# Kernel optimization log

Measured on AMD Instinct MI355X. Metric: run time of the kernel, lower is better.

Reference implementation:

```python
import jax, jax.numpy as jnp
import numpy as np

B, T, D, HD = 4, 4096, 1024, 64

def setup_inputs() -> dict:
    key = jax.random.key(0)
    kx, kq, kk, kv = jax.random.split(key, 4)
    s = 1.0 / np.sqrt(D)
    return {
        "x": jax.random.normal(kx, (B, T, D), dtype=jnp.float32),
        "wq": jax.random.uniform(kq, (HD, D), jnp.float32, -s, s),
        "wk": jax.random.uniform(kk, (HD, D), jnp.float32, -s, s),
        "wv": jax.random.uniform(kv, (HD, D), jnp.float32, -s, s),
    }

def reference(x, wq, wk, wv):
    # Linear(D, headDim, bias=False): y = x @ W.T with W of shape [headDim, D]
    Q = jnp.einsum('btD,dD->btd', x, wq)
    K = jnp.einsum('bsD,dD->bsd', x, wk)
    V = jnp.einsum('bsD,dD->bsd', x, wv)
    head_dim = wq.shape[0]
    logits = jnp.einsum('btd,bsd->bts', Q, K) / jnp.sqrt(jnp.float32(head_dim))
    attn = jax.nn.softmax(logits, axis=-1)
    return jnp.einsum('bts,bsd->btd', attn, V)
```

## Files before the change

### kernel.cpp

```cpp
#include <hip/hip_runtime.h>
#include <math.h>

#define TLEN 4096
#define BD   1024
#define HDIM 64
#define NB   4

typedef __attribute__((ext_vector_type(8))) short bf16x8;
typedef __attribute__((ext_vector_type(4))) float f32x4;
typedef __attribute__((ext_vector_type(16))) float f32x16;

__device__ __forceinline__ unsigned short f2bf(float f) {
    union { float f; unsigned u; } v; v.f = f;
    unsigned r = v.u + 0x7FFF + ((v.u >> 16) & 1);
    return (unsigned short)(r >> 16);
}

__device__ __forceinline__ unsigned cvt_pk_bf16(float lo, float hi) {
    unsigned r;
    asm("v_cvt_pk_bf16_f32 %0, %1, %2" : "=v"(r) : "v"(lo), "v"(hi));
    return r;
}

__device__ __forceinline__ bf16x8 cvt8pk(const float4 a, const float4 b) {
    union { unsigned u[4]; bf16x8 v; } r;
    r.u[0] = cvt_pk_bf16(a.x, a.y);
    r.u[1] = cvt_pk_bf16(a.z, a.w);
    r.u[2] = cvt_pk_bf16(b.x, b.y);
    r.u[3] = cvt_pk_bf16(b.z, b.w);
    return r.v;
}

__global__ __launch_bounds__(256) void wconv_kernel(
    const float* __restrict__ wq, const float* __restrict__ wk,
    const float* __restrict__ wv, unsigned short* __restrict__ wbf)
{
    const int r = blockIdx.x;
    const float* src = (r < 64) ? wq : (r < 128) ? wk : wv;
    const int rr = r & 63;
    const int c  = threadIdx.x * 4;
    float4 a = *(const float4*)&src[(size_t)rr * BD + c];
    uint2 o;
    o.x = cvt_pk_bf16(a.x, a.y);
    o.y = cvt_pk_bf16(a.z, a.w);
    *(uint2*)&wbf[(size_t)r * BD + c] = o;
}

__global__ __launch_bounds__(256, 2) void qkv_kernel(
    const float* __restrict__ x,
    const unsigned short* __restrict__ wbf,
    unsigned short* __restrict__ Qb,
    unsigned short* __restrict__ Kb,
    unsigned short* __restrict__ Vt)
{
    const int r0   = blockIdx.x * 32;
    const int tid  = threadIdx.x;
    const int lane = tid & 63;
    const int w    = tid >> 6;
    const int g    = lane >> 4;
    const int c    = lane & 15;

    __shared__ __align__(16) unsigned short wsh[2][192 * 64];
    __shared__ __align__(16) unsigned short xh[2][32 * 64];
    __shared__ __align__(16) unsigned short vtr[64][40];

    f32x4 acc[3][2];
    #pragma unroll
    for (int t = 0; t < 3; ++t)
        #pragma unroll
        for (int rg = 0; rg < 2; ++rg) acc[t][rg] = (f32x4){0.f, 0.f, 0.f, 0.f};

    uint4 wreg[6], xreg[2];
    const int xrow = tid >> 3;
    const int xpch = tid & 7;
    const int xgch = xpch ^ (xrow & 7);

    #define LOAD_W(k0s)                                                         \
        {                                                                       \
            _Pragma("unroll")                                                   \
            for (int ii = 0; ii < 6; ++ii) {                                    \
                const int L   = ii * 256 + tid;                                 \
                const int row = L >> 3;                                         \
                const int jl  = (L & 7) ^ (row & 7);                            \
                wreg[ii] = *(const uint4*)&wbf[(size_t)row * BD + (k0s) + jl * 8]; \
            }                                                                   \
        }
    #define WRITE_W(buf)                                                        \
        {                                                                       \
            _Pragma("unroll")                                                   \
            for (int ii = 0; ii < 6; ++ii) {                                    \
                const int L = ii * 256 + tid;                                   \
                *(uint4*)&wsh[buf][L * 8] = wreg[ii];                           \
            }                                                                   \
        }
    #define LOAD_X(k0s)                                                         \
        {                                                                       \
            const float* xs = &x[(size_t)(r0 + xrow) * BD + (k0s) + xgch * 8];  \
            xreg[0] = *(const uint4*)&xs[0];                                    \
            xreg[1] = *(const uint4*)&xs[4];                                    \
        }
    #define WRITE_X(buf)                                                        \
        {                                                                       \
            union { uint4 u; float4 f; } a0, a1;                                \
            a0.u = xreg[0]; a1.u = xreg[1];                                     \
            *(bf16x8*)&xh[buf][xrow * 64 + xpch * 8] = cvt8pk(a0.f, a1.f);      \
        }

    LOAD_W(0)
    LOAD_X(0)
    WRITE_W(0)
    WRITE_X(0)

    for (int it = 0; it < 16; ++it) {
        const int cb = it & 1;
        __syncthreads();

        if (it < 15) {
            LOAD_W((it + 1) * 64)
            LOAD_X((it + 1) * 64)
        }

        #pragma unroll
        for (int h = 0; h < 2; ++h) {
            const int oct = h * 4 + g;
            const int slot = (oct ^ (c & 7)) * 8;
            bf16x8 aX[2], bW[3];
            #pragma unroll
            for (int rg = 0; rg < 2; ++rg) {
                const int row = rg * 16 + c;
                aX[rg] = *(const bf16x8*)&xh[cb][row * 64 + slot];
            }
            #pragma unroll
            for (int t = 0; t < 3; ++t)
                bW[t] = *(const bf16x8*)&wsh[cb][((w * 3 + t) * 16 + c) * 64 + slot];
            #pragma unroll
            for (int t = 0; t < 3; ++t)
                #pragma unroll
                for (int rg = 0; rg < 2; ++rg)
                    acc[t][rg] = __builtin_amdgcn_mfma_f32_16x16x32_bf16(
                        aX[rg], bW[t], acc[t][rg], 0, 0, 0);
        }

        if (it < 15) {
            WRITE_W(cb ^ 1)
            WRITE_X(cb ^ 1)
        }
    }

    const float qscale = 0.18033688f;
    const int   bb     = r0 / TLEN;
    const int   trow   = r0 % TLEN;
    #pragma unroll
    for (int t = 0; t < 3; ++t) {
        const int m = w * 3 + t;
        #pragma unroll
        for (int rg = 0; rg < 2; ++rg)
            #pragma unroll
            for (int i = 0; i < 4; ++i) {
                const int row = rg * 16 + g * 4 + i;
                if (m < 4)
                    Qb[(size_t)(r0 + row) * HDIM + m * 16 + c]
                        = f2bf(acc[t][rg][i] * qscale);
                else if (m < 8)
                    Kb[(size_t)(r0 + row) * HDIM + (m - 4) * 16 + c]
                        = f2bf(acc[t][rg][i]);
                else
                    vtr[(m - 8) * 16 + c][row] = f2bf(acc[t][rg][i]);
            }
    }
    __syncthreads();
    {
        const int d    = tid >> 2;
        const int part = tid & 3;
        uint4 v0 = *(const uint4*)&vtr[d][part * 8];
        unsigned short* dst = Vt + (size_t)bb * HDIM * TLEN + (size_t)d * TLEN
                            + trow + part * 8;
        *(uint4*)&dst[0] = v0;
    }
    #undef LOAD_W
    #undef WRITE_W
    #undef LOAD_X
    #undef WRITE_X
}

template <int KEYS>
__global__ __launch_bounds__(256, 2) void attn_kernel(
    const unsigned short* __restrict__ Qb,
    const unsigned short* __restrict__ Kb,
    const unsigned short* __restrict__ Vt,
    float* __restrict__ O1, float* __restrict__ Ml, float* __restrict__ out)
{
    const int b     = blockIdx.y;
    const int q0    = blockIdx.x * 128;
    const int split = blockIdx.z;
    const int sbase = split * KEYS;

    const unsigned short* Qp = Qb + (size_t)b * TLEN * HDIM;
    const unsigned short* Kp = Kb + (size_t)b * TLEN * HDIM + (size_t)sbase * HDIM;
    const unsigned short* Vp = Vt + (size_t)b * HDIM * TLEN + sbase;

    const int tid  = threadIdx.x;
    const int lane = tid & 63;
    const int w    = tid >> 6;
    const int ql   = lane & 31;
    const int hi   = lane >> 5;
    const int ch   = lane & 7;

    __shared__ __align__(16) unsigned short ksh[2][4096];
    __shared__ __align__(16) unsigned short vsh[2][4096];

    bf16x8 qB[4];
    #pragma unroll
    for (int s = 0; s < 4; ++s)
        qB[s] = *(const bf16x8*)
            &Qp[(size_t)(q0 + w * 32 + ql) * HDIM + s * 16 + hi * 8];

    float  lsum = 0.f;
    f32x16 oacc[2];
    #pragma unroll
    for (int dt = 0; dt < 2; ++dt)
        #pragma unroll
        for (int i = 0; i < 16; ++i) oacc[dt][i] = 0.f;

    const int nt = KEYS / 64;

    uint4 kreg[2], vreg[2];
    #define LOAD_KV(s0)                                                         \
        {                                                                       \
            _Pragma("unroll")                                                   \
            for (int ii = 0; ii < 2; ++ii) {                                    \
                const int L   = ii * 256 + tid;                                 \
                const int row = L >> 3;                                         \
                const int jl  = (L & 7) ^ (row & 7);                            \
                kreg[ii] = *(const uint4*)&Kp[(size_t)((s0) + row) * HDIM + jl * 8]; \
                vreg[ii] = *(const uint4*)&Vp[(size_t)row * TLEN + (s0) + jl * 8];   \
            }                                                                   \
        }
    #define WRITE_KV(buf)                                                       \
        {                                                                       \
            _Pragma("unroll")                                                   \
            for (int ii = 0; ii < 2; ++ii) {                                    \
                const int L = ii * 256 + tid;                                   \
                *(uint4*)&ksh[buf][L * 8] = kreg[ii];                           \
                *(uint4*)&vsh[buf][L * 8] = vreg[ii];                           \
            }                                                                   \
        }

    LOAD_KV(0)
    WRITE_KV(0)

    for (int it = 0; it < nt; ++it) {
        const int cb = it & 1;
        __syncthreads();

        if (it + 1 < nt) LOAD_KV((it + 1) * 64)

        f32x16 sacc[2];
        #pragma unroll
        for (int kt = 0; kt < 2; ++kt)
            #pragma unroll
            for (int i = 0; i < 16; ++i) sacc[kt][i] = 0.f;
        __builtin_amdgcn_s_setprio(1);
        #pragma unroll
        for (int kt = 0; kt < 2; ++kt)
            #pragma unroll
            for (int s = 0; s < 4; ++s) {
                const bf16x8 kA = *(const bf16x8*)
                    &ksh[cb][(32 * kt + ql) * 64 + ((2 * s + hi) ^ ch) * 8];
                sacc[kt] = __builtin_amdgcn_mfma_f32_32x32x16_bf16(
                    kA, qB[s], sacc[kt], 0, 0, 0);
            }
        __builtin_amdgcn_s_setprio(0);

        if (it + 1 < nt) WRITE_KV(cb ^ 1)

        bf16x8 paf[4];
        #pragma unroll
        for (int kt = 0; kt < 2; ++kt) {
            float p[16];
            #pragma unroll
            for (int i = 0; i < 16; ++i)
                p[i] = __builtin_amdgcn_exp2f(sacc[kt][i]);
            lsum += (((p[0] + p[1]) + (p[2] + p[3]))
                   + ((p[4] + p[5]) + (p[6] + p[7])))
                  + (((p[8] + p[9]) + (p[10] + p[11]))
                   + ((p[12] + p[13]) + (p[14] + p[15])));
            #pragma unroll
            for (int bb = 0; bb < 2; ++bb) {
                const unsigned X0 = cvt_pk_bf16(p[8 * bb + 0], p[8 * bb + 1]);
                const unsigned X1 = cvt_pk_bf16(p[8 * bb + 2], p[8 * bb + 3]);
                const unsigned Z0 = cvt_pk_bf16(p[8 * bb + 4], p[8 * bb + 5]);
                const unsigned Z1 = cvt_pk_bf16(p[8 * bb + 6], p[8 * bb + 7]);
                auto s02 = __builtin_amdgcn_permlane32_swap(X0, Z0, false, false);
                auto s13 = __builtin_amdgcn_permlane32_swap(X1, Z1, false, false);
                union { unsigned u[4]; bf16x8 v; } pu;
                pu.u[0] = s02[0]; pu.u[1] = s13[0];
                pu.u[2] = s02[1]; pu.u[3] = s13[1];
                paf[kt * 2 + bb] = pu.v;
            }
        }

        __builtin_amdgcn_s_setprio(1);
        #pragma unroll
        for (int dt = 0; dt < 2; ++dt)
            #pragma unroll
            for (int s = 0; s < 4; ++s) {
                const bf16x8 vB = *(const bf16x8*)
                    &vsh[cb][(32 * dt + ql) * 64 + ((2 * s + hi) ^ ch) * 8];
                oacc[dt] = __builtin_amdgcn_mfma_f32_32x32x16_bf16(
                    paf[s], vB, oacc[dt], 0, 0, 0);
            }
        __builtin_amdgcn_s_setprio(0);
    }
    #undef LOAD_KV
    #undef WRITE_KV

    lsum += __shfl_xor(lsum, 32);

    if (KEYS == TLEN) {
        #pragma unroll
        for (int r = 0; r < 16; ++r) {
            const int   qr   = (r & 3) + 8 * (r >> 2) + 4 * hi;
            const float inv  = 1.0f / __shfl(lsum, qr);
            const size_t orow = (size_t)b * TLEN + q0 + w * 32 + qr;
            out[orow * HDIM + ql]      = oacc[0][r] * inv;
            out[orow * HDIM + 32 + ql] = oacc[1][r] * inv;
        }
    } else {
        float* Od = (split == 0)
            ? out : O1 + (size_t)(split - 1) * NB * TLEN * HDIM;
        #pragma unroll
        for (int r = 0; r < 16; ++r) {
            const int   qr   = (r & 3) + 8 * (r >> 2) + 4 * hi;
            const size_t orow = (size_t)b * TLEN + q0 + w * 32 + qr;
            Od[orow * HDIM + ql]      = oacc[0][r];
            Od[orow * HDIM + 32 + ql] = oacc[1][r];
        }
        if (lane < 32)
            Ml[(size_t)(split * NB + b) * TLEN + q0 + w * 32 + lane] = lsum;
    }
}

__global__ __launch_bounds__(256) void merge_kernel(
    float* __restrict__ out, const float* __restrict__ O1,
    const float* __restrict__ Ml)
{
    const int idx  = blockIdx.x * 256 + threadIdx.x;
    const int row  = idx >> 4;
    const int col4 = (idx & 15) * 4;
    const int b    = row >> 12;
    const int t    = row & (TLEN - 1);
    float l = 0.f;
    #pragma unroll
    for (int s = 0; s < 4; ++s) l += Ml[(size_t)(s * NB + b) * TLEN + t];
    const float inv = 1.0f / l;
    float4 a = *(const float4*)&out[(size_t)row * HDIM + col4];
    #pragma unroll
    for (int s = 1; s < 4; ++s) {
        float4 p = *(const float4*)
            &O1[(size_t)(s - 1) * NB * TLEN * HDIM + (size_t)row * HDIM + col4];
        a.x += p.x; a.y += p.y; a.z += p.z; a.w += p.w;
    }
    a.x *= inv; a.y *= inv; a.z *= inv; a.w *= inv;
    *(float4*)&out[(size_t)row * HDIM + col4] = a;
}

extern "C" void kernel_launch(void* const* d_in, const int* in_sizes, int n_in,
                              void* d_out, int out_size, void* d_ws, size_t ws_size,
                              hipStream_t stream)
{
    (void)in_sizes; (void)n_in; (void)out_size;
    const float* x  = (const float*)d_in[0];
    const float* wq = (const float*)d_in[1];
    const float* wk = (const float*)d_in[2];
    const float* wv = (const float*)d_in[3];
    float* out = (float*)d_out;

    unsigned short* wbf = (unsigned short*)d_out;
    unsigned short* Qbf = (unsigned short*)d_ws;
    unsigned short* Kbf = Qbf + (size_t)NB * TLEN * HDIM;
    unsigned short* Vtb = Kbf + (size_t)NB * TLEN * HDIM;
    float* Ml = (float*)((char*)d_ws + (size_t)3 * NB * TLEN * HDIM * 2);
    float* O1 = Ml + (size_t)4 * NB * TLEN;
    const size_t ws_need = (size_t)3 * NB * TLEN * HDIM * 2
                         + (size_t)4 * NB * TLEN * 4
                         + (size_t)3 * NB * TLEN * HDIM * 4;
    const bool use_split = ws_size >= ws_need;

    wconv_kernel<<<dim3(192), 256, 0, stream>>>(wq, wk, wv, wbf);
    qkv_kernel<<<dim3(NB * TLEN / 32), 256, 0, stream>>>(x, wbf, Qbf, Kbf, Vtb);

    if (use_split) {
        attn_kernel<TLEN / 4><<<dim3(TLEN / 128, NB, 4), 256, 0, stream>>>(
            Qbf, Kbf, Vtb, O1, Ml, out);
        merge_kernel<<<dim3(NB * TLEN * 16 / 256), 256, 0, stream>>>(out, O1, Ml);
    } else {
        attn_kernel<TLEN><<<dim3(TLEN / 128, NB, 1), 256, 0, stream>>>(
            Qbf, Kbf, Vtb, O1, Ml, out);
    }
}
```

Baseline: 138.5 us.

## Prefetch x two stages ahead and use non-draining barrier in QKV projection

The QKV projection kernel now keeps two register sets for x tiles and issues x global loads two iterations ahead, alternating between them in a fully unrolled loop. __syncthreads is replaced by a barrier that waits only on LDS counters (lgkmcnt), so outstanding global loads are not drained at each barrier. This is meant to hide the fp32 x load latency behind more compute. In exchange it uses more registers, which could pressure occupancy at launch bounds (256,2).

Result: no change. 139.7 us (+0.8%).

```diff
diff --git a/kernel.cpp b/kernel.cpp
--- a/kernel.cpp
+++ b/kernel.cpp
@@ -29,6 +29,13 @@
     r.u[2] = cvt_pk_bf16(b.x, b.y);
     r.u[3] = cvt_pk_bf16(b.z, b.w);
     return r.v;
+}
+
+__device__ __forceinline__ void sync_nodrain() {
+    asm volatile("s_waitcnt lgkmcnt(0)" ::: "memory");
+    __builtin_amdgcn_sched_barrier(0);
+    __builtin_amdgcn_s_barrier();
+    __builtin_amdgcn_sched_barrier(0);
 }
 
 __global__ __launch_bounds__(256) void wconv_kernel(
@@ -70,7 +77,8 @@
         #pragma unroll
         for (int rg = 0; rg < 2; ++rg) acc[t][rg] = (f32x4){0.f, 0.f, 0.f, 0.f};
 
-    uint4 wreg[6], xreg[2];
+    uint4 wreg[6];
+    uint4 xA0, xA1, xB0, xB1;
     const int xrow = tid >> 3;
     const int xpch = tid & 7;
     const int xgch = xpch ^ (xrow & 7);
@@ -93,58 +101,78 @@
                 *(uint4*)&wsh[buf][L * 8] = wreg[ii];                           \
             }                                                                   \
         }
-    #define LOAD_X(k0s)                                                         \
+    #define LOAD_XA(k0s)                                                        \
         {                                                                       \
             const float* xs = &x[(size_t)(r0 + xrow) * BD + (k0s) + xgch * 8];  \
-            xreg[0] = *(const uint4*)&xs[0];                                    \
-            xreg[1] = *(const uint4*)&xs[4];                                    \
-        }
-    #define WRITE_X(buf)                                                        \
+            xA0 = *(const uint4*)&xs[0];                                        \
+            xA1 = *(const uint4*)&xs[4];                                        \
+        }
+    #define LOAD_XB(k0s)                                                        \
+        {                                                                       \
+            const float* xs = &x[(size_t)(r0 + xrow) * BD + (k0s) + xgch * 8];  \
+            xB0 = *(const uint4*)&xs[0];                                        \
+            xB1 = *(const uint4*)&xs[4];                                        \
+        }
+    #define WRITE_XA(buf)                                                       \
         {                                                                       \
             union { uint4 u; float4 f; } a0, a1;                                \
-            a0.u = xreg[0]; a1.u = xreg[1];                                     \
+            a0.u = xA0; a1.u = xA1;                                             \
             *(bf16x8*)&xh[buf][xrow * 64 + xpch * 8] = cvt8pk(a0.f, a1.f);      \
         }
+    #define WRITE_XB(buf)                                                       \
+        {                                                                       \
+            union { uint4 u; float4 f; } a0, a1;                                \
+            a0.u = xB0; a1.u = xB1;                                             \
+            *(bf16x8*)&xh[buf][xrow * 64 + xpch * 8] = cvt8pk(a0.f, a1.f);      \
+        }
+
+    #define COMPUTE(cbv)                                                        \
+        {                                                                       \
+            _Pragma("unroll")                                                   \
+            for (int h = 0; h < 2; ++h) {                                       \
+                const int oct = h * 4 + g;                                      \
+                const int slot = (oct ^ (c & 7)) * 8;                           \
+                bf16x8 aX[2], bW[3];                                            \
+                _Pragma("unroll")                                               \
+                for (int rg = 0; rg < 2; ++rg) {                                \
+                    const int row = rg * 16 + c;                                \
+                    aX[rg] = *(const bf16x8*)&xh[cbv][row * 64 + slot];         \
+                }                                                               \
+                _Pragma("unroll")                                               \
+                for (int t = 0; t < 3; ++t)                                     \
+                    bW[t] = *(const bf16x8*)                                    \
+                        &wsh[cbv][((w * 3 + t) * 16 + c) * 64 + slot];          \
+                _Pragma("unroll")                                               \
+                for (int t = 0; t < 3; ++t)                                     \
+                    _Pragma("unroll")                                           \
+                    for (int rg = 0; rg < 2; ++rg)                              \
+                        acc[t][rg] = __builtin_amdgcn_mfma_f32_16x16x32_bf16(   \
+                            aX[rg], bW[t], acc[t][rg], 0, 0, 0);                \
+            }                                                                   \
+        }
+
+    #define QKV_BODY(itv, cbv, LOADXN, WRITEXC)                                 \
+        {                                                                       \
+            sync_nodrain();                                                     \
+            if ((itv) < 15) LOAD_W(((itv) + 1) * 64)                            \
+            if ((itv) < 14) LOADXN(((itv) + 2) * 64)                            \
+            COMPUTE(cbv)                                                        \
+            if ((itv) < 15) {                                                   \
+                WRITE_W((cbv) ^ 1)                                              \
+                WRITEXC((cbv) ^ 1)                                              \
+            }                                                                   \
+        }
 
     LOAD_W(0)
-    LOAD_X(0)
+    LOAD_XB(0)
     WRITE_W(0)
-    WRITE_X(0)
-
-    for (int it = 0; it < 16; ++it) {
-        const int cb = it & 1;
-        __syncthreads();
-
-        if (it < 15) {
-            LOAD_W((it + 1) * 64)
-            LOAD_X((it + 1) * 64)
-        }
-
-        #pragma unroll
-        for (int h = 0; h < 2; ++h) {
-            const int oct = h * 4 + g;
-            const int slot = (oct ^ (c & 7)) * 8;
-            bf16x8 aX[2], bW[3];
-            #pragma unroll
-            for (int rg = 0; rg < 2; ++rg) {
-                const int row = rg * 16 + c;
-                aX[rg] = *(const bf16x8*)&xh[cb][row * 64 + slot];
-            }
-            #pragma unroll
-            for (int t = 0; t < 3; ++t)
-                bW[t] = *(const bf16x8*)&wsh[cb][((w * 3 + t) * 16 + c) * 64 + slot];
-            #pragma unroll
-            for (int t = 0; t < 3; ++t)
-                #pragma unroll
-                for (int rg = 0; rg < 2; ++rg)
-                    acc[t][rg] = __builtin_amdgcn_mfma_f32_16x16x32_bf16(
-                        aX[rg], bW[t], acc[t][rg], 0, 0, 0);
-        }
-
-        if (it < 15) {
-            WRITE_W(cb ^ 1)
-            WRITE_X(cb ^ 1)
-        }
+    WRITE_XB(0)
+    LOAD_XA(64)
+
+    #pragma unroll
+    for (int it2 = 0; it2 < 8; ++it2) {
+        QKV_BODY(2 * it2,     0, LOAD_XB, WRITE_XA)
+        QKV_BODY(2 * it2 + 1, 1, LOAD_XA, WRITE_XB)
     }
 
     const float qscale = 0.18033688f;
@@ -179,8 +207,12 @@
     }
     #undef LOAD_W
     #undef WRITE_W
-    #undef LOAD_X
-    #undef WRITE_X
+    #undef LOAD_XA
+    #undef LOAD_XB
+    #undef WRITE_XA
+    #undef WRITE_XB
+    #undef COMPUTE
+    #undef QKV_BODY
 }
 
 template <int KEYS>
```

## Halve QKV projection row tile and single-buffer weights to raise occupancy

Applied to the files above, without the earlier changes.

The QKV projection kernel now handles 16 rows per block instead of 32, doubling the grid. The weight tile in shared memory drops from double to single buffering with an extra barrier, and launch bounds rise to 4 blocks per CU to cut LDS and register use and increase occupancy. In exchange, each block reloads the full 192x1024 weight slice for half as many rows, doubling weight traffic, and pays an extra barrier per iteration.

Measured after the change: 283.1 us. 2.04x slower.

```diff
diff --git a/kernel.cpp b/kernel.cpp
--- a/kernel.cpp
+++ b/kernel.cpp
@@ -46,34 +46,33 @@
     *(uint2*)&wbf[(size_t)r * BD + c] = o;
 }
 
-__global__ __launch_bounds__(256, 2) void qkv_kernel(
+__global__ __launch_bounds__(256, 4) void qkv_kernel(
     const float* __restrict__ x,
     const unsigned short* __restrict__ wbf,
     unsigned short* __restrict__ Qb,
     unsigned short* __restrict__ Kb,
     unsigned short* __restrict__ Vt)
 {
-    const int r0   = blockIdx.x * 32;
+    const int r0   = blockIdx.x * 16;
     const int tid  = threadIdx.x;
     const int lane = tid & 63;
     const int w    = tid >> 6;
     const int g    = lane >> 4;
     const int c    = lane & 15;
 
-    __shared__ __align__(16) unsigned short wsh[2][192 * 64];
-    __shared__ __align__(16) unsigned short xh[2][32 * 64];
-    __shared__ __align__(16) unsigned short vtr[64][40];
-
-    f32x4 acc[3][2];
-    #pragma unroll
-    for (int t = 0; t < 3; ++t)
-        #pragma unroll
-        for (int rg = 0; rg < 2; ++rg) acc[t][rg] = (f32x4){0.f, 0.f, 0.f, 0.f};
-
-    uint4 wreg[6], xreg[2];
-    const int xrow = tid >> 3;
-    const int xpch = tid & 7;
-    const int xgch = xpch ^ (xrow & 7);
+    __shared__ __align__(16) unsigned short wsh[192 * 64];
+    __shared__ __align__(16) unsigned short xh[2][16 * 64];
+    __shared__ __align__(16) unsigned short vtr[64][24];
+
+    f32x4 acc[3];
+    #pragma unroll
+    for (int t = 0; t < 3; ++t) acc[t] = (f32x4){0.f, 0.f, 0.f, 0.f};
+
+    uint4 wreg[6], xreg;
+    const int xrow  = tid >> 4;
+    const int xch   = (tid & 15) >> 1;
+    const int xhalf = tid & 1;
+    const int xgch  = xch ^ (xrow & 7);
 
     #define LOAD_W(k0s)                                                         \
         {                                                                       \
@@ -85,30 +84,32 @@
                 wreg[ii] = *(const uint4*)&wbf[(size_t)row * BD + (k0s) + jl * 8]; \
             }                                                                   \
         }
-    #define WRITE_W(buf)                                                        \
+    #define WRITE_W()                                                           \
         {                                                                       \
             _Pragma("unroll")                                                   \
             for (int ii = 0; ii < 6; ++ii) {                                    \
                 const int L = ii * 256 + tid;                                   \
-                *(uint4*)&wsh[buf][L * 8] = wreg[ii];                           \
+                *(uint4*)&wsh[L * 8] = wreg[ii];                                \
             }                                                                   \
         }
     #define LOAD_X(k0s)                                                         \
         {                                                                       \
-            const float* xs = &x[(size_t)(r0 + xrow) * BD + (k0s) + xgch * 8];  \
-            xreg[0] = *(const uint4*)&xs[0];                                    \
-            xreg[1] = *(const uint4*)&xs[4];                                    \
+            xreg = *(const uint4*)&x[(size_t)(r0 + xrow) * BD + (k0s)           \
+                                     + xgch * 8 + xhalf * 4];                   \
         }
     #define WRITE_X(buf)                                                        \
         {                                                                       \
-            union { uint4 u; float4 f; } a0, a1;                                \
-            a0.u = xreg[0]; a1.u = xreg[1];                                     \
-            *(bf16x8*)&xh[buf][xrow * 64 + xpch * 8] = cvt8pk(a0.f, a1.f);      \
+            union { uint4 u; float4 f; } a0;                                    \
+            a0.u = xreg;                                                        \
+            uint2 o;                                                            \
+            o.x = cvt_pk_bf16(a0.f.x, a0.f.y);                                  \
+            o.y = cvt_pk_bf16(a0.f.z, a0.f.w);                                  \
+            *(uint2*)&xh[buf][xrow * 64 + xch * 8 + xhalf * 4] = o;             \
         }
 
     LOAD_W(0)
     LOAD_X(0)
-    WRITE_W(0)
+    WRITE_W()
     WRITE_X(0)
 
     for (int it = 0; it < 16; ++it) {
@@ -124,27 +125,21 @@
         for (int h = 0; h < 2; ++h) {
             const int oct = h * 4 + g;
             const int slot = (oct ^ (c & 7)) * 8;
-            bf16x8 aX[2], bW[3];
-            #pragma unroll
-            for (int rg = 0; rg < 2; ++rg) {
-                const int row = rg * 16 + c;
-                aX[rg] = *(const bf16x8*)&xh[cb][row * 64 + slot];
-            }
+            bf16x8 bW[3];
+            const bf16x8 aX = *(const bf16x8*)&xh[cb][c * 64 + slot];
             #pragma unroll
             for (int t = 0; t < 3; ++t)
-                bW[t] = *(const bf16x8*)&wsh[cb][((w * 3 + t) * 16 + c) * 64 + slot];
+                bW[t] = *(const bf16x8*)&wsh[((w * 3 + t) * 16 + c) * 64 + slot];
             #pragma unroll
             for (int t = 0; t < 3; ++t)
-                #pragma unroll
-                for (int rg = 0; rg < 2; ++rg)
-                    acc[t][rg] = __builtin_amdgcn_mfma_f32_16x16x32_bf16(
-                        aX[rg], bW[t], acc[t][rg], 0, 0, 0);
-        }
-
-        if (it < 15) {
-            WRITE_W(cb ^ 1)
-            WRITE_X(cb ^ 1)
-        }
+                acc[t] = __builtin_amdgcn_mfma_f32_16x16x32_bf16(
+                    aX, bW[t], acc[t], 0, 0, 0);
+        }
+
+        if (it < 15) WRITE_X(cb ^ 1)
+
+        __syncthreads();
+        if (it < 15) WRITE_W()
     }
 
     const float qscale = 0.18033688f;
@@ -154,28 +149,26 @@
     for (int t = 0; t < 3; ++t) {
         const int m = w * 3 + t;
         #pragma unroll
-        for (int rg = 0; rg < 2; ++rg)
-            #pragma unroll
-            for (int i = 0; i < 4; ++i) {
-                const int row = rg * 16 + g * 4 + i;
-                if (m < 4)
-                    Qb[(size_t)(r0 + row) * HDIM + m * 16 + c]
-                        = f2bf(acc[t][rg][i] * qscale);
-                else if (m < 8)
-                    Kb[(size_t)(r0 + row) * HDIM + (m - 4) * 16 + c]
-                        = f2bf(acc[t][rg][i]);
-                else
-                    vtr[(m - 8) * 16 + c][row] = f2bf(acc[t][rg][i]);
-            }
+        for (int i = 0; i < 4; ++i) {
+            const int row = g * 4 + i;
+            if (m < 4)
+                Qb[(size_t)(r0 + row) * HDIM + m * 16 + c]
+                    = f2bf(acc[t][i] * qscale);
+            else if (m < 8)
+                Kb[(size_t)(r0 + row) * HDIM + (m - 4) * 16 + c]
+                    = f2bf(acc[t][i]);
+            else
+                vtr[(m - 8) * 16 + c][row] = f2bf(acc[t][i]);
+        }
     }
     __syncthreads();
     {
         const int d    = tid >> 2;
         const int part = tid & 3;
-        uint4 v0 = *(const uint4*)&vtr[d][part * 8];
+        uint2 v0 = *(const uint2*)&vtr[d][part * 4];
         unsigned short* dst = Vt + (size_t)bb * HDIM * TLEN + (size_t)d * TLEN
-                            + trow + part * 8;
-        *(uint4*)&dst[0] = v0;
+                            + trow + part * 4;
+        *(uint2*)&dst[0] = v0;
     }
     #undef LOAD_W
     #undef WRITE_W
@@ -388,7 +381,7 @@
     const bool use_split = ws_size >= ws_need;
 
     wconv_kernel<<<dim3(192), 256, 0, stream>>>(wq, wk, wv, wbf);
-    qkv_kernel<<<dim3(NB * TLEN / 32), 256, 0, stream>>>(x, wbf, Qbf, Kbf, Vtb);
+    qkv_kernel<<<dim3(NB * TLEN / 16), 256, 0, stream>>>(x, wbf, Qbf, Kbf, Vtb);
 
     if (use_split) {
         attn_kernel<TLEN / 4><<<dim3(TLEN / 128, NB, 4), 256, 0, stream>>>(
```
